# Performance work log

Measured on AMD Instinct MI355X. Metric: run time of the kernel, lower is better.

Reference implementation:

```python
import jax, jax.numpy as jnp
import numpy as np

D_MODEL = 1024
NUM_HEADS = 16
D_K = D_MODEL // NUM_HEADS


def setup_inputs() -> dict:
    key = jax.random.key(0)
    ks = jax.random.split(key, 9)
    B, S = 4, 2048
    s = 1.0 / np.sqrt(D_MODEL)
    inp = {
        "x": jax.random.normal(ks[0], (B, S, D_MODEL), dtype=jnp.float32),
        "wq": jax.random.uniform(ks[1], (D_MODEL, D_MODEL), jnp.float32, -s, s),
        "bq": jax.random.uniform(ks[2], (D_MODEL,), jnp.float32, -s, s),
        "wk": jax.random.uniform(ks[3], (D_MODEL, D_MODEL), jnp.float32, -s, s),
        "bk": jax.random.uniform(ks[4], (D_MODEL,), jnp.float32, -s, s),
        "wv": jax.random.uniform(ks[5], (D_MODEL, D_MODEL), jnp.float32, -s, s),
        "bv": jax.random.uniform(ks[6], (D_MODEL,), jnp.float32, -s, s),
        "wo": jax.random.uniform(ks[7], (D_MODEL, D_MODEL), jnp.float32, -s, s),
        "bo": jax.random.uniform(ks[8], (D_MODEL,), jnp.float32, -s, s),
    }
    return inp


def reference(x, wq, bq, wk, bk, wv, bv, wo, bo):
    B, S, _ = x.shape
    H, Dk = NUM_HEADS, D_K
    # QKV projections; weights stored as (in, out) so y = x @ w + b
    q = (x @ wq + bq).reshape(B, S, H, Dk).transpose(0, 2, 1, 3)  # (B,H,S,Dk)
    k = (x @ wk + bk).reshape(B, S, H, Dk).transpose(0, 2, 1, 3)
    v = (x @ wv + bv).reshape(B, S, H, Dk).transpose(0, 2, 1, 3)
    scores = jnp.einsum("bhqd,bhkd->bhqk", q, k) / jnp.sqrt(jnp.float32(Dk))
    causal = jnp.tril(jnp.ones((S, S), dtype=bool))  # True = keep
    scores = jnp.where(causal, scores, jnp.float32(-jnp.inf))
    attn = jax.nn.softmax(scores, axis=-1)  # dropout=0 (eval)
    out = jnp.einsum("bhqk,bhkd->bhqd", attn, v)
    out = out.transpose(0, 2, 1, 3).reshape(B, S, H * Dk)
    return out @ wo + bo
```

## Files before the change

### kernel.cpp

```cpp
#include <hip/hip_runtime.h>
#include <hip/hip_bf16.h>


#define D_MODEL 1024
#define NHEADS  16
#define DK      64
#define BATCH   4
#define SEQ     2048
#define MROWS   (BATCH*SEQ)

typedef short bvec8 __attribute__((ext_vector_type(8)));
typedef float fvec4  __attribute__((ext_vector_type(4)));
typedef float fvec16 __attribute__((ext_vector_type(16)));

__device__ __forceinline__ unsigned short f2bf(float f) {
    unsigned int x = __float_as_uint(f);
    x += 0x7fffu + ((x >> 16) & 1u);
    return (unsigned short)(x >> 16);
}

__device__ __forceinline__ unsigned pack_bf16x2(float a, float b) {
#if __has_builtin(__builtin_amdgcn_cvt_pk_bf16_f32)
    typedef __bf16 bf16x2_t __attribute__((ext_vector_type(2)));
    union { bf16x2_t v; unsigned u; } cv;
    cv.v = __builtin_amdgcn_cvt_pk_bf16_f32(a, b);
    return cv.u;
#else
    return (unsigned)f2bf(a) | ((unsigned)f2bf(b) << 16);
#endif
}

__device__ __forceinline__ float fast_exp2(float x) {
#if __has_builtin(__builtin_amdgcn_exp2f)
    return __builtin_amdgcn_exp2f(x);
#else
    return exp2f(x);
#endif
}


__global__ void f32_to_bf16_k(const float* __restrict__ in,
                              unsigned short* __restrict__ out, int n4) {
    int i = blockIdx.x * 256 + threadIdx.x;
    if (i < n4) {
        float4 v = ((const float4*)in)[i];
        ushort4 o;
        o.x = f2bf(v.x); o.y = f2bf(v.y); o.z = f2bf(v.z); o.w = f2bf(v.w);
        ((ushort4*)out)[i] = o;
    }
}

__global__ void transpose_all_k(const float* __restrict__ wq, const float* __restrict__ wk,
                                const float* __restrict__ wv, const float* __restrict__ wo,
                                unsigned short* __restrict__ wqkvt,
                                unsigned short* __restrict__ wot) {
    __shared__ float tile[32][33];
    const int z = blockIdx.z;
    const float* W = (z == 0) ? wq : (z == 1) ? wk : (z == 2) ? wv : wo;
    unsigned short* Wt = (z == 3) ? wot : wqkvt + (size_t)z * D_MODEL * D_MODEL;
    int n0 = blockIdx.x * 32, k0 = blockIdx.y * 32;
    int tx = threadIdx.x & 31;
    int ty = (threadIdx.x >> 5) * 4;
#pragma unroll
    for (int i = 0; i < 4; ++i)
        tile[ty + i][tx] = W[(k0 + ty + i) * D_MODEL + n0 + tx];
    __syncthreads();
#pragma unroll
    for (int i = 0; i < 4; ++i)
        Wt[(n0 + ty + i) * D_MODEL + k0 + tx] = f2bf(tile[tx][ty + i]);
}

__global__ void build_cbias_k(const float* __restrict__ bq, const float* __restrict__ bk,
                              const float* __restrict__ bv, float* __restrict__ cb) {
    int i = blockIdx.x * 256 + threadIdx.x;
    float v = (i < 1024) ? bq[i] : (i < 2048) ? bk[i - 1024] : bv[i - 2048];
    cb[i] = v;
}

__global__ __launch_bounds__(256, 2)
void gemm_glds(const unsigned short* __restrict__ A,
               const unsigned short* __restrict__ Bt,
               const float* __restrict__ bias,
               unsigned short* __restrict__ oq,
               unsigned short* __restrict__ ok,
               unsigned short* __restrict__ ov,
               float* __restrict__ of,
               float qscale, int mode) {
    __shared__ __align__(16) unsigned short As[2][128 * 64];
    __shared__ __align__(16) unsigned short Bs[2][128 * 64];

    const int tid  = threadIdx.x;
    const int lane = tid & 63;
    const int w    = tid >> 6;
    const int wr   = w >> 1, wc = w & 1;
    const int quad = lane >> 4, l16 = lane & 15;
    const int rowBlock = blockIdx.y * 128;
    const int colBlock = blockIdx.x * 128;

    const int lrow   = lane >> 3;
    const int gchunk = (lane & 7) ^ lrow;

    fvec4 acc[4][4] = {};

    {
#pragma unroll
        for (int n = 0; n < 4; ++n) {
            const int g = w * 4 + n;
            __builtin_amdgcn_global_load_lds(
                (const __attribute__((address_space(1))) void*)
                    &A[(size_t)(rowBlock + g * 8 + lrow) * D_MODEL + gchunk * 8],
                (__attribute__((address_space(3))) void*)&As[0][g * 512], 16, 0, 0);
            __builtin_amdgcn_global_load_lds(
                (const __attribute__((address_space(1))) void*)
                    &Bt[(size_t)(colBlock + g * 8 + lrow) * D_MODEL + gchunk * 8],
                (__attribute__((address_space(3))) void*)&Bs[0][g * 512], 16, 0, 0);
        }
    }

    for (int i = 0; i < 16; ++i) {
        __syncthreads();
        const int buf = i & 1;
        if (i < 15) {
            const int k1 = (i + 1) * 64;
#pragma unroll
            for (int n = 0; n < 4; ++n) {
                const int g = w * 4 + n;
                __builtin_amdgcn_global_load_lds(
                    (const __attribute__((address_space(1))) void*)
                        &A[(size_t)(rowBlock + g * 8 + lrow) * D_MODEL + k1 + gchunk * 8],
                    (__attribute__((address_space(3))) void*)&As[buf ^ 1][g * 512], 16, 0, 0);
                __builtin_amdgcn_global_load_lds(
                    (const __attribute__((address_space(1))) void*)
                        &Bt[(size_t)(colBlock + g * 8 + lrow) * D_MODEL + k1 + gchunk * 8],
                    (__attribute__((address_space(3))) void*)&Bs[buf ^ 1][g * 512], 16, 0, 0);
            }
        }
#pragma unroll
        for (int kc = 0; kc < 2; ++kc) {
            bvec8 af[4], bfr[4];
#pragma unroll
            for (int ii = 0; ii < 4; ++ii) {
                int r = wr * 64 + ii * 16 + l16;
                af[ii] = *(const bvec8*)&As[buf][r * 64 + (((kc * 4 + quad) ^ (l16 & 7)) * 8)];
            }
#pragma unroll
            for (int j = 0; j < 4; ++j) {
                int r = wc * 64 + j * 16 + l16;
                bfr[j] = *(const bvec8*)&Bs[buf][r * 64 + (((kc * 4 + quad) ^ (l16 & 7)) * 8)];
            }
#pragma unroll
            for (int ii = 0; ii < 4; ++ii)
#pragma unroll
                for (int j = 0; j < 4; ++j)
                    acc[ii][j] = __builtin_amdgcn_mfma_f32_16x16x32_bf16(
                        af[ii], bfr[j], acc[ii][j], 0, 0, 0);
        }
    }

    if (mode == 0) {
#pragma unroll
        for (int i = 0; i < 4; ++i) {
#pragma unroll
            for (int j = 0; j < 4; ++j) {
                int ncol = colBlock + wc * 64 + j * 16 + l16;
                int which = ncol >> 10;
                int nn = ncol & 1023;
                int h = nn >> 6, d = nn & 63;
                float bv = bias[ncol];
#pragma unroll
                for (int r = 0; r < 4; ++r) {
                    int mrow = rowBlock + wr * 64 + i * 16 + quad * 4 + r;
                    int b = mrow >> 11, s = mrow & (SEQ - 1);
                    float v = acc[i][j][r] + bv;
                    if (which == 0)
                        oq[(((b * NHEADS + h) * SEQ + s) * DK) + d] = f2bf(v * qscale);
                    else if (which == 1)
                        ok[(((b * NHEADS + h) * SEQ + s) * DK) + d] = f2bf(v);
                    else
                        ov[(((b * NHEADS + h) * DK + d) * SEQ) + s] = f2bf(v);
                }
            }
        }
    } else {
#pragma unroll
        for (int i = 0; i < 4; ++i) {
#pragma unroll
            for (int j = 0; j < 4; ++j) {
                int ncol = colBlock + wc * 64 + j * 16 + l16;
                float bv = bias[ncol];
#pragma unroll
                for (int r = 0; r < 4; ++r) {
                    int mrow = rowBlock + wr * 64 + i * 16 + quad * 4 + r;
                    of[(size_t)mrow * D_MODEL + ncol] = acc[i][j][r] + bv;
                }
            }
        }
    }
}

__global__ __launch_bounds__(256, 4)
void attn_mfma8(const unsigned short* __restrict__ Q,
                const unsigned short* __restrict__ K,
                const unsigned short* __restrict__ Vt,
                unsigned short* __restrict__ O) {
    __shared__ __align__(16) unsigned short Ksm[2][64 * 64];
    __shared__ __align__(16) unsigned short Vsm[2][64 * 64];
    __shared__ float Lsh[4][32];

    const int tid  = threadIdx.x;
    const int lane = tid & 63;
    const int wq   = tid >> 6;
    const int hf   = lane >> 5;
    const int l32  = lane & 31;
    const int bx = blockIdx.x;
    const int qt = (bx & 1) ? ((bx - 1) >> 1) : (15 - (bx >> 1));
    const int hh = blockIdx.y, b = blockIdx.z;

    const size_t bhq = ((size_t)b * NHEADS + hh) * SEQ * DK;
    const unsigned short* Qb = Q + bhq;
    const unsigned short* Kb = K + bhq;
    const unsigned short* Vb = Vt + bhq;

    const int q0 = qt * 128 + wq * 32;

    bvec8 qf[4];
#pragma unroll
    for (int kc = 0; kc < 4; ++kc)
        qf[kc] = *(const bvec8*)&Qb[(q0 + l32) * DK + kc * 16 + hf * 8];

    const int sr = tid >> 2;
    const int sc = tid & 3;
    const int sp0 = ((sc) ^ (sr & 7)) * 8;
    const int sp1 = ((sc + 4) ^ (sr & 7)) * 8;

    const int ktmax = 2 * qt + 1;
    const int ktact = 2 * qt + (wq >> 1);
    const int mofs  = (wq & 1) << 5;

    bvec8 kr0, kr1, vr0, vr1;
    {
        const unsigned short* kg = Kb + sr * DK;
        kr0 = *(const bvec8*)(kg + sc * 8);
        kr1 = *(const bvec8*)(kg + (sc + 4) * 8);
        const unsigned short* vg = Vb + sr * SEQ;
        vr0 = *(const bvec8*)(vg + sc * 8);
        vr1 = *(const bvec8*)(vg + (sc + 4) * 8);
        *(bvec8*)&Ksm[0][sr * 64 + sp0] = kr0;
        *(bvec8*)&Ksm[0][sr * 64 + sp1] = kr1;
        *(bvec8*)&Vsm[0][sr * 64 + sp0] = vr0;
        *(bvec8*)&Vsm[0][sr * 64 + sp1] = vr1;
    }

    fvec16 acc0 = {};
    fvec16 acc1 = {};
    float lp = 0.f;

    for (int kt = 0; kt <= ktmax; ++kt) {
        __syncthreads();
        const int buf = kt & 1;
        if (kt < ktmax) {
            const unsigned short* kg = Kb + ((kt + 1) * 64 + sr) * DK;
            kr0 = *(const bvec8*)(kg + sc * 8);
            kr1 = *(const bvec8*)(kg + (sc + 4) * 8);
            const unsigned short* vg = Vb + sr * SEQ + (kt + 1) * 64;
            vr0 = *(const bvec8*)(vg + sc * 8);
            vr1 = *(const bvec8*)(vg + (sc + 4) * 8);
        }
        if (kt <= ktact) {
            const unsigned short* Kbuf = &Ksm[buf][0];
            const unsigned short* Vbuf = &Vsm[buf][0];

            fvec16 s0 = {}, s1 = {};
#pragma unroll
            for (int kc = 0; kc < 4; ++kc) {
                const int ch = (((kc * 2 + hf) ^ (l32 & 7)) * 8);
                bvec8 a0 = *(const bvec8*)&Kbuf[l32 * 64 + ch];
                bvec8 a1 = *(const bvec8*)&Kbuf[(32 + l32) * 64 + ch];
                s0 = __builtin_amdgcn_mfma_f32_32x32x16_bf16(a0, qf[kc], s0, 0, 0, 0);
                s1 = __builtin_amdgcn_mfma_f32_32x32x16_bf16(a1, qf[kc], s1, 0, 0, 0);
            }

            if (kt == ktact) {
#pragma unroll
                for (int r = 0; r < 16; ++r) {
                    const int key0 = (r & 3) + 8 * (r >> 2) + 4 * hf - mofs;
                    if (key0 > l32)      s0[r] = -__builtin_inff();
                    if (key0 + 32 > l32) s1[r] = -__builtin_inff();
                }
            }

            unsigned pk[16];
#pragma unroll
            for (int m = 0; m < 8; ++m) {
                float p0 = fast_exp2(s0[2 * m]);
                float p1 = fast_exp2(s0[2 * m + 1]);
                float p2 = fast_exp2(s1[2 * m]);
                float p3 = fast_exp2(s1[2 * m + 1]);
                lp += (p0 + p1) + (p2 + p3);
                pk[m]     = pack_bf16x2(p0, p1);
                pk[8 + m] = pack_bf16x2(p2, p3);
            }

#pragma unroll
            for (int kc16 = 0; kc16 < 4; ++kc16) {
                const int b0 = (kc16 >> 1) * 8 + (kc16 & 1) * 4;
                unsigned sw0 = __shfl_xor(pk[b0 + 0], 32);
                unsigned sw1 = __shfl_xor(pk[b0 + 1], 32);
                unsigned sw2 = __shfl_xor(pk[b0 + 2], 32);
                unsigned sw3 = __shfl_xor(pk[b0 + 3], 32);
                union { unsigned u[4]; bvec8 v; } afu;
                afu.u[0] = hf ? sw2 : pk[b0 + 0];
                afu.u[1] = hf ? sw3 : pk[b0 + 1];
                afu.u[2] = hf ? pk[b0 + 2] : sw0;
                afu.u[3] = hf ? pk[b0 + 3] : sw1;
                const int ch = (((kc16 * 2 + hf) ^ (l32 & 7)) * 8);
                bvec8 bv0 = *(const bvec8*)&Vbuf[l32 * 64 + ch];
                bvec8 bv1 = *(const bvec8*)&Vbuf[(32 + l32) * 64 + ch];
                acc0 = __builtin_amdgcn_mfma_f32_32x32x16_bf16(afu.v, bv0, acc0, 0, 0, 0);
                acc1 = __builtin_amdgcn_mfma_f32_32x32x16_bf16(afu.v, bv1, acc1, 0, 0, 0);
            }
        }
        if (kt < ktmax) {
            const int nb = buf ^ 1;
            *(bvec8*)&Ksm[nb][sr * 64 + sp0] = kr0;
            *(bvec8*)&Ksm[nb][sr * 64 + sp1] = kr1;
            *(bvec8*)&Vsm[nb][sr * 64 + sp0] = vr0;
            *(bvec8*)&Vsm[nb][sr * 64 + sp1] = vr1;
        }
    }

    {
        float l = lp + __shfl_xor(lp, 32);
        if (lane < 32) Lsh[wq][l32] = l;
    }
#pragma unroll
    for (int g = 0; g < 4; ++g) {
        float4 lv = *(const float4*)&Lsh[wq][g * 8 + 4 * hf];
#pragma unroll
        for (int rr = 0; rr < 4; ++rr) {
            const int reg = g * 4 + rr;
            const int qrow = q0 + g * 8 + 4 * hf + rr;
            const float inv = 1.f / ((const float*)&lv)[rr];
            unsigned short* dst = O + (size_t)(b * SEQ + qrow) * D_MODEL + hh * DK + l32;
            dst[0]  = f2bf(acc0[reg] * inv);
            dst[32] = f2bf(acc1[reg] * inv);
        }
    }
}


extern "C" void kernel_launch(void* const* d_in, const int* in_sizes, int n_in,
                              void* d_out, int out_size, void* d_ws, size_t ws_size,
                              hipStream_t stream) {
    const float* x  = (const float*)d_in[0];
    const float* wq = (const float*)d_in[1];
    const float* bq = (const float*)d_in[2];
    const float* wk = (const float*)d_in[3];
    const float* bk = (const float*)d_in[4];
    const float* wv = (const float*)d_in[5];
    const float* bv = (const float*)d_in[6];
    const float* wo = (const float*)d_in[7];
    const float* bo = (const float*)d_in[8];
    float* out = (float*)d_out;

    char* ws = (char*)d_ws;
    const size_t MB = 1u << 20;
    unsigned short* xb    = (unsigned short*)(ws);
    unsigned short* wqkvt = (unsigned short*)(ws + 16 * MB);
    unsigned short* wot   = (unsigned short*)(ws + 22 * MB);
    unsigned short* qb    = (unsigned short*)(ws + 24 * MB);
    unsigned short* kb    = (unsigned short*)(ws + 40 * MB);
    unsigned short* vtb   = (unsigned short*)(ws + 56 * MB);
    unsigned short* ab    = (unsigned short*)(ws + 72 * MB);
    float* cbias = (float*)(ws + 72 * MB);

    f32_to_bf16_k<<<(MROWS * D_MODEL / 4 + 255) / 256, 256, 0, stream>>>(
        x, xb, MROWS * D_MODEL / 4);
    transpose_all_k<<<dim3(32, 32, 4), 256, 0, stream>>>(wq, wk, wv, wo, wqkvt, wot);
    build_cbias_k<<<12, 256, 0, stream>>>(bq, bk, bv, cbias);

    const float QSCALE = 0.125f * 1.44269504088896340736f;

    gemm_glds<<<dim3(3072 / 128, MROWS / 128), 256, 0, stream>>>(
        xb, wqkvt, cbias, qb, kb, vtb, nullptr, QSCALE, 0);

    attn_mfma8<<<dim3(SEQ / 128, NHEADS, BATCH), 256, 0, stream>>>(qb, kb, vtb, ab);

    gemm_glds<<<dim3(D_MODEL / 128, MROWS / 128), 256, 0, stream>>>(
        ab, wot, bo, nullptr, nullptr, nullptr, out, 1.0f, 1);
}
```

Measured before the change: 310.2 us.

## Split KV range of longest causal query tiles and merge with combine kernel

The five heaviest causal query tiles per head are each split into two blocks covering disjoint KV ranges. Each block writes unnormalized fp32 partial outputs and row sums to workspace, and a new combine kernel adds them, normalizes and writes bf16. The goal is to shorten the long-tail blocks that dominate the causal attention grid and improve load balance across CUs. In exchange it adds an extra kernel launch and about 20 MB of fp32 partial-result traffic. The workspace it uses overlaps buffers that are already consumed by the time attention runs.

```diff
diff --git a/kernel.cpp b/kernel.cpp
--- a/kernel.cpp
+++ b/kernel.cpp
@@ -199,10 +199,12 @@
 }
 
 __global__ __launch_bounds__(256, 4)
-void attn_mfma8(const unsigned short* __restrict__ Q,
+void attn_mfma9(const unsigned short* __restrict__ Q,
                 const unsigned short* __restrict__ K,
                 const unsigned short* __restrict__ Vt,
-                unsigned short* __restrict__ O) {
+                unsigned short* __restrict__ O,
+                float* __restrict__ Opart,
+                float* __restrict__ Lpart) {
     __shared__ __align__(16) unsigned short Ksm[2][64 * 64];
     __shared__ __align__(16) unsigned short Vsm[2][64 * 64];
     __shared__ float Lsh[4][32];
@@ -212,11 +214,24 @@
     const int wq   = tid >> 6;
     const int hf   = lane >> 5;
     const int l32  = lane & 31;
+    const int hh = blockIdx.y, b = blockIdx.z;
+    const int hb = b * NHEADS + hh;
+
     const int bx = blockIdx.x;
-    const int qt = (bx & 1) ? ((bx - 1) >> 1) : (15 - (bx >> 1));
-    const int hh = blockIdx.y, b = blockIdx.z;
-
-    const size_t bhq = ((size_t)b * NHEADS + hh) * SEQ * DK;
+    int qt, kt0, kt1, slot;
+    bool part;
+    if (bx < 10) {
+        qt   = 15 - (bx >> 1);
+        const int half = bx & 1;
+        slot = (qt - 11) * 2 + half;
+        part = true;
+        if (half == 0) { kt0 = 0;  kt1 = 17; }
+        else           { kt0 = 17; kt1 = 2 * qt + 2; }
+    } else {
+        qt = 20 - bx; kt0 = 0; kt1 = 2 * qt + 2; part = false; slot = 0;
+    }
+
+    const size_t bhq = ((size_t)hb) * SEQ * DK;
     const unsigned short* Qb = Q + bhq;
     const unsigned short* Kb = K + bhq;
     const unsigned short* Vb = Vt + bhq;
@@ -233,16 +248,15 @@
     const int sp0 = ((sc) ^ (sr & 7)) * 8;
     const int sp1 = ((sc + 4) ^ (sr & 7)) * 8;
 
-    const int ktmax = 2 * qt + 1;
     const int ktact = 2 * qt + (wq >> 1);
     const int mofs  = (wq & 1) << 5;
 
     bvec8 kr0, kr1, vr0, vr1;
     {
-        const unsigned short* kg = Kb + sr * DK;
+        const unsigned short* kg = Kb + (kt0 * 64 + sr) * DK;
         kr0 = *(const bvec8*)(kg + sc * 8);
         kr1 = *(const bvec8*)(kg + (sc + 4) * 8);
-        const unsigned short* vg = Vb + sr * SEQ;
+        const unsigned short* vg = Vb + sr * SEQ + kt0 * 64;
         vr0 = *(const bvec8*)(vg + sc * 8);
         vr1 = *(const bvec8*)(vg + (sc + 4) * 8);
         *(bvec8*)&Ksm[0][sr * 64 + sp0] = kr0;
@@ -255,10 +269,10 @@
     fvec16 acc1 = {};
     float lp = 0.f;
 
-    for (int kt = 0; kt <= ktmax; ++kt) {
+    for (int kt = kt0; kt < kt1; ++kt) {
         __syncthreads();
-        const int buf = kt & 1;
-        if (kt < ktmax) {
+        const int buf = (kt - kt0) & 1;
+        if (kt + 1 < kt1) {
             const unsigned short* kg = Kb + ((kt + 1) * 64 + sr) * DK;
             kr0 = *(const bvec8*)(kg + sc * 8);
             kr1 = *(const bvec8*)(kg + (sc + 4) * 8);
@@ -320,8 +334,8 @@
                 acc1 = __builtin_amdgcn_mfma_f32_32x32x16_bf16(afu.v, bv1, acc1, 0, 0, 0);
             }
         }
-        if (kt < ktmax) {
-            const int nb = buf ^ 1;
+        if (kt + 1 < kt1) {
+            const int nb = ((kt - kt0) & 1) ^ 1;
             *(bvec8*)&Ksm[nb][sr * 64 + sp0] = kr0;
             *(bvec8*)&Ksm[nb][sr * 64 + sp1] = kr1;
             *(bvec8*)&Vsm[nb][sr * 64 + sp0] = vr0;
@@ -329,22 +343,55 @@
         }
     }
 
-    {
-        float l = lp + __shfl_xor(lp, 32);
+    const float l = lp + __shfl_xor(lp, 32);
+
+    if (part) {
+        if (lane < 32)
+            Lpart[((size_t)slot * 64 + hb) * 128 + wq * 32 + l32] = l;
+        float* Od = Opart + (((size_t)slot * 64 + hb) * 128 + wq * 32) * 64;
+#pragma unroll
+        for (int g = 0; g < 4; ++g)
+#pragma unroll
+            for (int rr = 0; rr < 4; ++rr) {
+                const int reg = g * 4 + rr;
+                const int qrl = g * 8 + 4 * hf + rr;
+                Od[(size_t)qrl * 64 + l32]      = acc0[reg];
+                Od[(size_t)qrl * 64 + 32 + l32] = acc1[reg];
+            }
+    } else {
         if (lane < 32) Lsh[wq][l32] = l;
-    }
-#pragma unroll
-    for (int g = 0; g < 4; ++g) {
-        float4 lv = *(const float4*)&Lsh[wq][g * 8 + 4 * hf];
-#pragma unroll
-        for (int rr = 0; rr < 4; ++rr) {
-            const int reg = g * 4 + rr;
-            const int qrow = q0 + g * 8 + 4 * hf + rr;
-            const float inv = 1.f / ((const float*)&lv)[rr];
-            unsigned short* dst = O + (size_t)(b * SEQ + qrow) * D_MODEL + hh * DK + l32;
-            dst[0]  = f2bf(acc0[reg] * inv);
-            dst[32] = f2bf(acc1[reg] * inv);
-        }
+#pragma unroll
+        for (int g = 0; g < 4; ++g) {
+            float4 lv = *(const float4*)&Lsh[wq][g * 8 + 4 * hf];
+#pragma unroll
+            for (int rr = 0; rr < 4; ++rr) {
+                const int reg = g * 4 + rr;
+                const int qrow = q0 + g * 8 + 4 * hf + rr;
+                const float inv = 1.f / ((const float*)&lv)[rr];
+                unsigned short* dst = O + (size_t)(b * SEQ + qrow) * D_MODEL + hh * DK + l32;
+                dst[0]  = f2bf(acc0[reg] * inv);
+                dst[32] = f2bf(acc1[reg] * inv);
+            }
+        }
+    }
+}
+
+__global__ void attn_combine_k(const float* __restrict__ Opart,
+                               const float* __restrict__ Lpart,
+                               unsigned short* __restrict__ O) {
+    const int qt = 11 + blockIdx.x;
+    const int h = blockIdx.y, b = blockIdx.z;
+    const int hb = b * NHEADS + h;
+    const int s0 = (qt - 11) * 2;
+    const float* A  = Opart + ((size_t)(s0)*64 + hb) * 128 * 64;
+    const float* Bp = Opart + ((size_t)(s0 + 1) * 64 + hb) * 128 * 64;
+    const float* LA = Lpart + ((size_t)(s0)*64 + hb) * 128;
+    const float* LB = Lpart + ((size_t)(s0 + 1) * 64 + hb) * 128;
+    for (int e = threadIdx.x; e < 128 * 64; e += 256) {
+        const int qr = e >> 6, d = e & 63;
+        const float inv = 1.f / (LA[qr] + LB[qr]);
+        const float v = (A[e] + Bp[e]) * inv;
+        O[(size_t)(b * SEQ + qt * 128 + qr) * D_MODEL + h * DK + d] = f2bf(v);
     }
 }
 
@@ -373,6 +420,8 @@
     unsigned short* vtb   = (unsigned short*)(ws + 56 * MB);
     unsigned short* ab    = (unsigned short*)(ws + 72 * MB);
     float* cbias = (float*)(ws + 72 * MB);
+    float* Opart = (float*)(ws);
+    float* Lpart = (float*)(ws + 21 * MB);
 
     f32_to_bf16_k<<<(MROWS * D_MODEL / 4 + 255) / 256, 256, 0, stream>>>(
         x, xb, MROWS * D_MODEL / 4);
@@ -384,7 +433,9 @@
     gemm_glds<<<dim3(3072 / 128, MROWS / 128), 256, 0, stream>>>(
         xb, wqkvt, cbias, qb, kb, vtb, nullptr, QSCALE, 0);
 
-    attn_mfma8<<<dim3(SEQ / 128, NHEADS, BATCH), 256, 0, stream>>>(qb, kb, vtb, ab);
+    attn_mfma9<<<dim3(21, NHEADS, BATCH), 256, 0, stream>>>(
+        qb, kb, vtb, ab, Opart, Lpart);
+    attn_combine_k<<<dim3(5, NHEADS, BATCH), 256, 0, stream>>>(Opart, Lpart, ab);
 
     gemm_glds<<<dim3(D_MODEL / 128, MROWS / 128), 256, 0, stream>>>(
         ab, wot, bo, nullptr, nullptr, nullptr, out, 1.0f, 1);
```

Result: faster. 296.5 us (-4.4%).
